# Kernel optimization log

Hardware: AMD Instinct MI355X
Metric: run time of the kernel (lower is better)

## Reference

```python
import jax, jax.numpy as jnp
import numpy as np

NUM_FREQ = 4
MAX_FREQ_LOG2 = 10.0
# standard NeRF frequency bands: 2^linspace(0, max_freq_log2, num_freq)
FREQ_BANDS = 2.0 ** np.linspace(0.0, MAX_FREQ_LOG2, NUM_FREQ).astype(np.float32)


def positional_encoding(x):
    # x: [N, 3] -> [N, 3*(1 + 2*num_freq)] = [N, 27]
    xf = x[..., None, :] * jnp.asarray(FREQ_BANDS, dtype=x.dtype)[:, None]  # [N, F, 3]
    enc = jnp.concatenate([jnp.sin(xf), jnp.cos(xf)], axis=-1)  # [N, F, 6]
    return jnp.concatenate([x, enc.reshape(x.shape[0], -1)], axis=-1)


def setup_inputs() -> dict:
    key = jax.random.key(0)
    k1, k2, k3 = jax.random.split(key, 3)
    N = 2097152
    x = jax.random.normal(k1, (N, 3), dtype=jnp.float32)
    in_dim, hidden = 27, 32
    # torch Linear default init scale ~ 1/sqrt(fan_in)
    W1 = jax.random.normal(k2, (in_dim, hidden), dtype=jnp.float32) / np.sqrt(in_dim)
    b1 = jnp.zeros((hidden,), dtype=jnp.float32)
    W2 = jax.random.normal(k3, (hidden, 1), dtype=jnp.float32) / np.sqrt(hidden)
    b2 = jnp.zeros((1,), dtype=jnp.float32)
    return {"x": x, "W1": W1, "b1": b1, "W2": W2, "b2": b2}


def reference(x, W1, b1, W2, b2):
    t = positional_encoding(x)                    # [N, 27]
    h = jax.nn.relu(t @ W1 + b1)                  # [N, 32]
    out = jax.nn.relu(h @ W2 + b2)                # [N, 1]
    return out
```

## Files before the change

### kernel.cpp

```cpp
#include <hip/hip_runtime.h>


#define NPTS  2097152
#define BLOCK 256
#define TILES 4
#define NBLK  (NPTS / (BLOCK * TILES))
#define TROW  40

typedef __bf16 bf16x8 __attribute__((ext_vector_type(8)));
typedef float  f32x4  __attribute__((ext_vector_type(4)));
typedef float  f32x2  __attribute__((ext_vector_type(2)));

__global__ __launch_bounds__(BLOCK, 4) void nerf_mfma3(
    const float* __restrict__ x,
    const float* __restrict__ W1,
    const float* __restrict__ b1,
    const float* __restrict__ W2,
    const float* __restrict__ b2,
    float* __restrict__ out)
{
    __shared__ __bf16 tbuf[4][64 * TROW];

    const int tid  = threadIdx.x;
    const int wave = tid >> 6;
    const int lane = tid & 63;
    const int g    = lane >> 4;
    const int c    = lane & 15;

    bf16x8 afrag[2];
    #pragma unroll
    for (int mt = 0; mt < 2; ++mt) {
        const int j = mt * 16 + c;
        #pragma unroll
        for (int i = 0; i < 8; ++i) {
            const int k = g * 8 + i;
            float v = 0.0f;
            if (k < 27)       v = W1[k * 32 + j];
            else if (k == 27) v = b1[j];
            afrag[mt][i] = (__bf16)v;
        }
    }
    f32x2 w2p[2][2];
    #pragma unroll
    for (int mt = 0; mt < 2; ++mt)
        #pragma unroll
        for (int rr = 0; rr < 2; ++rr) {
            w2p[mt][rr][0] = W2[mt * 16 + g * 4 + 2 * rr + 0];
            w2p[mt][rr][1] = W2[mt * 16 + g * 4 + 2 * rr + 1];
        }
    const float bias2 = b2[0];

    const float Fr[4] = {
        0.15915494309189535f,
        10.079368f * 0.15915494309189535f,
        101.59367f * 0.15915494309189535f,
        1024.0f    * 0.15915494309189535f
    };

    const int tbase = blockIdx.x * (4 * TILES) + wave * TILES;

    float nx0, nx1, nx2;
    {
        const int p0 = tbase * 64 + lane;
        nx0 = x[p0 * 3 + 0]; nx1 = x[p0 * 3 + 1]; nx2 = x[p0 * 3 + 2];
    }

    #pragma unroll
    for (int t = 0; t < TILES; ++t) {
        const float x0 = nx0, x1 = nx1, x2 = nx2;
        if (t + 1 < TILES) {
            const int pn = (tbase + t + 1) * 64 + lane;
            nx0 = x[pn * 3 + 0]; nx1 = x[pn * 3 + 1]; nx2 = x[pn * 3 + 2];
        }

        bf16x8 tch[4] = {};
#define TSET(idx, val) tch[(idx) / 8][(idx) % 8] = (__bf16)(val)
        TSET(0, x0); TSET(1, x1); TSET(2, x2);
        #pragma unroll
        for (int f = 0; f < 4; ++f) {
            const float r0 = x0 * Fr[f], r1 = x1 * Fr[f], r2 = x2 * Fr[f];
            const float a0 = r0 - floorf(r0);
            const float a1 = r1 - floorf(r1);
            const float a2 = r2 - floorf(r2);
            TSET(3 + 6 * f + 0, __builtin_amdgcn_sinf(a0));
            TSET(3 + 6 * f + 1, __builtin_amdgcn_sinf(a1));
            TSET(3 + 6 * f + 2, __builtin_amdgcn_sinf(a2));
            TSET(3 + 6 * f + 3, __builtin_amdgcn_cosf(a0));
            TSET(3 + 6 * f + 4, __builtin_amdgcn_cosf(a1));
            TSET(3 + 6 * f + 5, __builtin_amdgcn_cosf(a2));
        }
        TSET(27, 1.0f);
#undef TSET

        __bf16* myrow = &tbuf[wave][lane * TROW];
        #pragma unroll
        for (int ch = 0; ch < 4; ++ch)
            *(bf16x8*)(myrow + ch * 8) = tch[ch];

        bf16x8 bfrag[4];
        #pragma unroll
        for (int nt = 0; nt < 4; ++nt)
            bfrag[nt] = *(bf16x8*)(&tbuf[wave][(nt * 16 + c) * TROW + g * 8]);

        f32x4 acc[4][2] = {};
        #pragma unroll
        for (int nt = 0; nt < 4; ++nt)
            #pragma unroll
            for (int mt = 0; mt < 2; ++mt)
                acc[nt][mt] = __builtin_amdgcn_mfma_f32_16x16x32_bf16(
                    afrag[mt], bfrag[nt], acc[nt][mt], 0, 0, 0);

        float p[4];
        #pragma unroll
        for (int nt = 0; nt < 4; ++nt) {
            f32x2 ps = {0.0f, 0.0f};
            #pragma unroll
            for (int mt = 0; mt < 2; ++mt)
                #pragma unroll
                for (int rr = 0; rr < 2; ++rr) {
                    f32x2 a;
                    a[0] = fmaxf(acc[nt][mt][2 * rr + 0], 0.0f);
                    a[1] = fmaxf(acc[nt][mt][2 * rr + 1], 0.0f);
                    ps = ps + a * w2p[mt][rr];
                }
            p[nt] = ps[0] + ps[1];
        }

        const bool hi2 = (g >= 2), odd = (g & 1);
        const float s0 = hi2 ? p[0] : p[2];
        const float s1 = hi2 ? p[1] : p[3];
        const float k0 = hi2 ? p[2] : p[0];
        const float k1 = hi2 ? p[3] : p[1];
        const float r0 = k0 + __shfl_xor(s0, 32, 64);
        const float r1 = k1 + __shfl_xor(s1, 32, 64);
        const float uk = odd ? r1 : r0;
        const float us = odd ? r0 : r1;
        const float S  = uk + __shfl_xor(us, 16, 64);

        out[(tbase + t) * 64 + lane] = fmaxf(S + bias2, 0.0f);
    }
}

extern "C" void kernel_launch(void* const* d_in, const int* in_sizes, int n_in,
                              void* d_out, int out_size, void* d_ws, size_t ws_size,
                              hipStream_t stream) {
    const float* x  = (const float*)d_in[0];
    const float* W1 = (const float*)d_in[1];
    const float* b1 = (const float*)d_in[2];
    const float* W2 = (const float*)d_in[3];
    const float* b2 = (const float*)d_in[4];
    float* out = (float*)d_out;

    nerf_mfma3<<<NBLK, BLOCK, 0, stream>>>(x, W1, b1, W2, b2, out);
}
```

Baseline: 21.32 us.

## Build MFMA B-fragments directly in registers, removing the LDS transpose

The K dimension of the first layer is reordered so that each 8-wide lane group g holds the sin/cos features of one frequency band plus one raw coordinate or the bias. Each lane can then compute its MFMA B operand directly in registers from x, with no LDS staging or transposing. Every lane now loads the x values of the 4 points it contributes (12 loads per tile instead of 3), and per-lane transcendental work drops from 24 to 24 evaluations spread across 4 points at one frequency, for the same total. This removes the LDS round trip, and range reduction uses fract. In exchange it adds redundant global loads of x across lane groups.

Result: faster. 20.09 us (-5.7%).

```diff
diff --git a/kernel.cpp b/kernel.cpp
--- a/kernel.cpp
+++ b/kernel.cpp
@@ -5,13 +5,12 @@
 #define BLOCK 256
 #define TILES 4
 #define NBLK  (NPTS / (BLOCK * TILES))
-#define TROW  40
 
 typedef __bf16 bf16x8 __attribute__((ext_vector_type(8)));
 typedef float  f32x4  __attribute__((ext_vector_type(4)));
 typedef float  f32x2  __attribute__((ext_vector_type(2)));
 
-__global__ __launch_bounds__(BLOCK, 4) void nerf_mfma3(
+__global__ __launch_bounds__(BLOCK, 4) void nerf_mfma4(
     const float* __restrict__ x,
     const float* __restrict__ W1,
     const float* __restrict__ b1,
@@ -19,27 +18,33 @@
     const float* __restrict__ b2,
     float* __restrict__ out)
 {
-    __shared__ __bf16 tbuf[4][64 * TROW];
-
     const int tid  = threadIdx.x;
     const int wave = tid >> 6;
     const int lane = tid & 63;
     const int g    = lane >> 4;
     const int c    = lane & 15;
 
+    const float INV2PI = 0.15915494309189535f;
+    float Fg = 1.0f;
+    Fg = (g == 1) ? 10.079368f : Fg;
+    Fg = (g == 2) ? 101.59367f : Fg;
+    Fg = (g == 3) ? 1024.0f    : Fg;
+    Fg *= INV2PI;
+
     bf16x8 afrag[2];
     #pragma unroll
     for (int mt = 0; mt < 2; ++mt) {
         const int j = mt * 16 + c;
         #pragma unroll
-        for (int i = 0; i < 8; ++i) {
-            const int k = g * 8 + i;
-            float v = 0.0f;
-            if (k < 27)       v = W1[k * 32 + j];
-            else if (k == 27) v = b1[j];
-            afrag[mt][i] = (__bf16)v;
-        }
+        for (int i = 0; i < 3; ++i)
+            afrag[mt][i] = (__bf16)W1[(3 + 6 * g + i) * 32 + j];
+        #pragma unroll
+        for (int i = 3; i < 6; ++i)
+            afrag[mt][i] = (__bf16)W1[(6 + 6 * g + (i - 3)) * 32 + j];
+        afrag[mt][6] = (__bf16)((g < 3) ? W1[g * 32 + j] : b1[j]);
+        afrag[mt][7] = (__bf16)0.0f;
     }
+
     f32x2 w2p[2][2];
     #pragma unroll
     for (int mt = 0; mt < 2; ++mt)
@@ -50,79 +55,69 @@
         }
     const float bias2 = b2[0];
 
-    const float Fr[4] = {
-        0.15915494309189535f,
-        10.079368f * 0.15915494309189535f,
-        101.59367f * 0.15915494309189535f,
-        1024.0f    * 0.15915494309189535f
-    };
-
     const int tbase = blockIdx.x * (4 * TILES) + wave * TILES;
 
-    float nx0, nx1, nx2;
+    float px[4][3], nx_[4][3];
     {
-        const int p0 = tbase * 64 + lane;
-        nx0 = x[p0 * 3 + 0]; nx1 = x[p0 * 3 + 1]; nx2 = x[p0 * 3 + 2];
+        const float* xb = x + (size_t)tbase * 192;
+        #pragma unroll
+        for (int nt = 0; nt < 4; ++nt)
+            #pragma unroll
+            for (int cm = 0; cm < 3; ++cm)
+                px[nt][cm] = xb[(16 * nt + c) * 3 + cm];
     }
 
     #pragma unroll
     for (int t = 0; t < TILES; ++t) {
-        const float x0 = nx0, x1 = nx1, x2 = nx2;
         if (t + 1 < TILES) {
-            const int pn = (tbase + t + 1) * 64 + lane;
-            nx0 = x[pn * 3 + 0]; nx1 = x[pn * 3 + 1]; nx2 = x[pn * 3 + 2];
+            const float* xb = x + (size_t)(tbase + t + 1) * 192;
+            #pragma unroll
+            for (int nt = 0; nt < 4; ++nt)
+                #pragma unroll
+                for (int cm = 0; cm < 3; ++cm)
+                    nx_[nt][cm] = xb[(16 * nt + c) * 3 + cm];
         }
-
-        bf16x8 tch[4] = {};
-#define TSET(idx, val) tch[(idx) / 8][(idx) % 8] = (__bf16)(val)
-        TSET(0, x0); TSET(1, x1); TSET(2, x2);
-        #pragma unroll
-        for (int f = 0; f < 4; ++f) {
-            const float r0 = x0 * Fr[f], r1 = x1 * Fr[f], r2 = x2 * Fr[f];
-            const float a0 = r0 - floorf(r0);
-            const float a1 = r1 - floorf(r1);
-            const float a2 = r2 - floorf(r2);
-            TSET(3 + 6 * f + 0, __builtin_amdgcn_sinf(a0));
-            TSET(3 + 6 * f + 1, __builtin_amdgcn_sinf(a1));
-            TSET(3 + 6 * f + 2, __builtin_amdgcn_sinf(a2));
-            TSET(3 + 6 * f + 3, __builtin_amdgcn_cosf(a0));
-            TSET(3 + 6 * f + 4, __builtin_amdgcn_cosf(a1));
-            TSET(3 + 6 * f + 5, __builtin_amdgcn_cosf(a2));
-        }
-        TSET(27, 1.0f);
-#undef TSET
-
-        __bf16* myrow = &tbuf[wave][lane * TROW];
-        #pragma unroll
-        for (int ch = 0; ch < 4; ++ch)
-            *(bf16x8*)(myrow + ch * 8) = tch[ch];
-
-        bf16x8 bfrag[4];
-        #pragma unroll
-        for (int nt = 0; nt < 4; ++nt)
-            bfrag[nt] = *(bf16x8*)(&tbuf[wave][(nt * 16 + c) * TROW + g * 8]);
-
-        f32x4 acc[4][2] = {};
-        #pragma unroll
-        for (int nt = 0; nt < 4; ++nt)
-            #pragma unroll
-            for (int mt = 0; mt < 2; ++mt)
-                acc[nt][mt] = __builtin_amdgcn_mfma_f32_16x16x32_bf16(
-                    afrag[mt], bfrag[nt], acc[nt][mt], 0, 0, 0);
 
         float p[4];
         #pragma unroll
         for (int nt = 0; nt < 4; ++nt) {
+            const float x0 = px[nt][0], x1 = px[nt][1], x2 = px[nt][2];
+
+            const float a0 = __builtin_amdgcn_fractf(x0 * Fg);
+            const float a1 = __builtin_amdgcn_fractf(x1 * Fg);
+            const float a2 = __builtin_amdgcn_fractf(x2 * Fg);
+            float extra = x0;
+            extra = (g == 1) ? x1 : extra;
+            extra = (g == 2) ? x2 : extra;
+            extra = (g == 3) ? 1.0f : extra;
+
+            bf16x8 bf;
+            bf[0] = (__bf16)__builtin_amdgcn_sinf(a0);
+            bf[1] = (__bf16)__builtin_amdgcn_sinf(a1);
+            bf[2] = (__bf16)__builtin_amdgcn_sinf(a2);
+            bf[3] = (__bf16)__builtin_amdgcn_cosf(a0);
+            bf[4] = (__bf16)__builtin_amdgcn_cosf(a1);
+            bf[5] = (__bf16)__builtin_amdgcn_cosf(a2);
+            bf[6] = (__bf16)extra;
+            bf[7] = (__bf16)0.0f;
+
+            f32x4 acc0 = {0.f, 0.f, 0.f, 0.f};
+            f32x4 acc1 = {0.f, 0.f, 0.f, 0.f};
+            acc0 = __builtin_amdgcn_mfma_f32_16x16x32_bf16(afrag[0], bf, acc0, 0, 0, 0);
+            acc1 = __builtin_amdgcn_mfma_f32_16x16x32_bf16(afrag[1], bf, acc1, 0, 0, 0);
+
             f32x2 ps = {0.0f, 0.0f};
             #pragma unroll
-            for (int mt = 0; mt < 2; ++mt)
-                #pragma unroll
-                for (int rr = 0; rr < 2; ++rr) {
-                    f32x2 a;
-                    a[0] = fmaxf(acc[nt][mt][2 * rr + 0], 0.0f);
-                    a[1] = fmaxf(acc[nt][mt][2 * rr + 1], 0.0f);
-                    ps = ps + a * w2p[mt][rr];
-                }
+            for (int rr = 0; rr < 2; ++rr) {
+                f32x2 a;
+                a[0] = fmaxf(acc0[2 * rr + 0], 0.0f);
+                a[1] = fmaxf(acc0[2 * rr + 1], 0.0f);
+                ps = ps + a * w2p[0][rr];
+                f32x2 b;
+                b[0] = fmaxf(acc1[2 * rr + 0], 0.0f);
+                b[1] = fmaxf(acc1[2 * rr + 1], 0.0f);
+                ps = ps + b * w2p[1][rr];
+            }
             p[nt] = ps[0] + ps[1];
         }
 
@@ -138,6 +133,12 @@
         const float S  = uk + __shfl_xor(us, 16, 64);
 
         out[(tbase + t) * 64 + lane] = fmaxf(S + bias2, 0.0f);
+
+        #pragma unroll
+        for (int nt = 0; nt < 4; ++nt)
+            #pragma unroll
+            for (int cm = 0; cm < 3; ++cm)
+                px[nt][cm] = nx_[nt][cm];
     }
 }
 
@@ -151,5 +152,5 @@
     const float* b2 = (const float*)d_in[4];
     float* out = (float*)d_out;
 
-    nerf_mfma3<<<NBLK, BLOCK, 0, stream>>>(x, W1, b1, W2, b2, out);
+    nerf_mfma4<<<NBLK, BLOCK, 0, stream>>>(x, W1, b1, W2, b2, out);
 }
```
